# Kernel optimization log

Measured on AMD Instinct MI355X. Metric: run time of the kernel, lower is better.

Reference implementation:

```python
import jax, jax.numpy as jnp
from jax import lax
import numpy as np

SEQ_LEN = 96; PRED_LEN = 96; SIGNAL_LEN = 16; NUM_NODES = 256
EMBED = 128; HIDDEN = 64; K_NN = 8; S_SCALE = 2.0; CHEB_ORDER = 2
MA_K = 3; BATCH = 16
C_FREQ = SIGNAL_LEN // 2 + 1          # 9 rfft bins
M_NODES = NUM_NODES * C_FREQ          # nodes per sample graph


def _sin_posemb(pos, dim):
    half = dim // 2
    freqs = 1.0 / (10000.0 ** (np.arange(half) / half))
    ang = pos[:, None] * freqs[None, :]
    return np.concatenate([np.sin(ang), np.cos(ang)], axis=-1).astype(np.float32)


def setup_inputs():
    key = jax.random.key(0)
    ks = jax.random.split(key, 12)
    x = jax.random.normal(ks[0], (BATCH, SEQ_LEN, NUM_NODES), jnp.float32)
    # Chebyshev (order 2) approx of Haar framelet filters cos(xi/2), sin(xi/2) on [0, pi]
    t = np.linspace(-1.0, 1.0, 201); xi = (t + 1.0) * np.pi / 2.0
    ch = np.polynomial.chebyshev
    approx = np.stack([ch.chebfit(t, np.cos(xi / 2.0), CHEB_ORDER),
                       ch.chebfit(t, np.sin(xi / 2.0), CHEB_ORDER)]).astype(np.float32)
    freq_emb = _sin_posemb(np.arange(C_FREQ, dtype=np.float32) * S_SCALE, EMBED)
    sc = (2.0 / EMBED) ** 0.5
    return dict(
        x=x,
        approx=jnp.asarray(approx),                 # [F=2, K=3]
        theta=jnp.ones((2,), jnp.float32),
        fr_Wr=jax.random.normal(ks[1], (EMBED, EMBED), jnp.float32) * sc,
        fr_Wi=jax.random.normal(ks[2], (EMBED, EMBED), jnp.float32) * sc,
        eo_Wr=jax.random.normal(ks[3], (1, EMBED), jnp.float32) * sc,
        eo_Wi=jax.random.normal(ks[4], (1, EMBED), jnp.float32) * sc,
        freq_emb=jnp.asarray(freq_emb),             # [C, EMBED]
        n1_w=jnp.ones((NUM_NODES,), jnp.float32), n1_b=jnp.zeros((NUM_NODES,), jnp.float32),
        n2_w=jnp.ones((NUM_NODES,), jnp.float32), n2_b=jnp.zeros((NUM_NODES,), jnp.float32),
        W1_w=jax.random.normal(ks[5], (HIDDEN, SEQ_LEN), jnp.float32) * (1.0 / SEQ_LEN ** 0.5),
        W1_b=jnp.zeros((HIDDEN,), jnp.float32),
        W2_w=jax.random.normal(ks[6], (HIDDEN, HIDDEN), jnp.float32) * (1.0 / HIDDEN ** 0.5),
        W2_b=jnp.zeros((HIDDEN,), jnp.float32),
        Wt_w=jax.random.normal(ks[7], (HIDDEN, SEQ_LEN), jnp.float32) * (1.0 / SEQ_LEN ** 0.5),
        Wt_b=jnp.zeros((HIDDEN,), jnp.float32),
        W3_w=jax.random.normal(ks[8], (PRED_LEN, HIDDEN), jnp.float32) * (1.0 / HIDDEN ** 0.5),
        W3_b=jnp.zeros((PRED_LEN,), jnp.float32),
    )


def _clinear(z, Wr, Wi):
    xr, xi = z.real, z.imag
    return lax.complex(xr @ Wr.T - xi @ Wi.T, xr @ Wi.T + xi @ Wr.T)


def _csilu(z):
    return lax.complex(jax.nn.silu(z.real), jax.nn.silu(z.imag))


def _cheb_prop(h, row, col, ew, coeffs):
    # Chebyshev recurrence with A_norm(h) = scatter_add(row, (ew/s) * h[col])
    w = (ew / S_SCALE)[:, None]
    def A(hh):
        return jnp.zeros_like(hh).at[row].add(w * hh[col])
    Tx0 = h
    out = coeffs[0] * Tx0
    Tx1 = -A(Tx0)
    out = out + coeffs[1] * Tx1
    for ki in range(2, CHEB_ORDER + 1):
        Tx2 = -2.0 * A(Tx1) - Tx0
        out = out + coeffs[ki] * Tx2
        Tx0, Tx1 = Tx1, Tx2
    return out


def _knn_one(feat):
    # feat [M, 2] -> symmetrised degree-normalised KNN edges
    sq = jnp.sum(feat * feat, axis=1)
    d2 = sq[:, None] + sq[None, :] - 2.0 * (feat @ feat.T)
    d2 = jnp.where(jnp.eye(M_NODES, dtype=bool), jnp.inf, d2)
    idx = lax.top_k(-d2, K_NN)[1]                      # smallest distances
    src = jnp.repeat(jnp.arange(M_NODES), K_NN)
    dst = idx.reshape(-1)
    r = jnp.concatenate([src, dst])
    c = jnp.concatenate([dst, src])
    deg = jnp.zeros((M_NODES,), jnp.float32).at[r].add(1.0)
    dinv = (deg + 1e-8) ** -0.5
    return r, c, dinv[r] * dinv[c]


def _moving_avg(x):
    pad = MA_K // 2
    front = jnp.repeat(x[:, :1, :], pad, axis=1)
    back = jnp.repeat(x[:, -1:, :], MA_K - 1 - pad, axis=1)
    xp = jnp.concatenate([front, x, back], axis=1)     # (B, T+k-1, N)
    cs = jnp.cumsum(xp, axis=1)
    cs = jnp.concatenate([jnp.zeros_like(cs[:, :1, :]), cs], axis=1)
    return (cs[:, MA_K:, :] - cs[:, :-MA_K, :]) / MA_K  # (B, T, N)


def _inorm(h, w, b):
    mu = jnp.mean(h, axis=-1, keepdims=True)
    var = jnp.mean((h - mu) ** 2, axis=-1, keepdims=True)
    return (h - mu) / jnp.sqrt(var + 1e-5) * w[None, :, None] + b[None, :, None]


def _forward(x, approx, theta, fr_Wr, fr_Wi, eo_Wr, eo_Wi, freq_emb,
             n1_w, n1_b, n2_w, n2_b, W1_w, W1_b, W2_w, W2_b, Wt_w, Wt_b, W3_w, W3_b):
    B, T, N = x.shape
    trend = _moving_avg(x)
    seasonal = x - trend
    S = jnp.fft.rfft(seasonal, n=SIGNAL_LEN, axis=1, norm='ortho')   # (B, C, N) c64
    S_perm = jnp.transpose(S, (0, 2, 1))                             # (B, N, C)
    node_feat = S_perm[..., None] * freq_emb                         # (B, N, C, E) c64
    batch_x = node_feat.reshape(B * M_NODES, EMBED)
    sg = S_perm.reshape(B, M_NODES)
    feat = lax.stop_gradient(jnp.stack([sg.real, sg.imag], axis=-1))  # (B, M, 2)
    rs, cs_, ews = jax.vmap(_knn_one)(feat)
    off = (jnp.arange(B) * M_NODES)[:, None]
    row = (rs + off).reshape(-1)
    col = (cs_ + off).reshape(-1)
    ew = ews.reshape(-1)
    # framelet layer: sum of F filtered Chebyshev propagations
    acc = jnp.zeros_like(batch_x)
    for i in range(approx.shape[0]):
        acc = acc + theta[i] * _cheb_prop(batch_x, row, col, ew, approx[i])
    h = _csilu(_clinear(acc, fr_Wr, fr_Wi))
    S_out = _clinear(h, eo_Wr, eo_Wi).reshape(B, N, C_FREQ)
    H = jnp.fft.irfft(jnp.transpose(S_out, (0, 2, 1)), n=SEQ_LEN, axis=1, norm='ortho')
    H = jnp.transpose(H, (0, 2, 1))                                  # (B, N, T)
    H = jax.nn.silu(_inorm(H, n1_w, n1_b))
    H = H @ W1_w.T + W1_b
    H = jax.nn.silu(_inorm(H, n2_w, n2_b))
    H = H @ W2_w.T + W2_b
    trend_emb = jnp.transpose(trend, (0, 2, 1)) @ Wt_w.T + Wt_b
    return (H + trend_emb) @ W3_w.T + W3_b                           # (B, N, pred_len)


def reference(x, approx, theta, fr_Wr, fr_Wi, eo_Wr, eo_Wi, freq_emb,
              n1_w, n1_b, n2_w, n2_b, W1_w, W1_b, W2_w, W2_b, Wt_w, Wt_b, W3_w, W3_b):
    return _forward(x, approx, theta, fr_Wr, fr_Wi, eo_Wr, eo_Wi, freq_emb,
                    n1_w, n1_b, n2_w, n2_b, W1_w, W1_b, W2_w, W2_b, Wt_w, Wt_b, W3_w, W3_b)
```

## Files before the change

kernel.cpp:

```cpp
#include <hip/hip_runtime.h>
#include <math.h>
#include <float.h>

#define BATCH 16
#define SEQ 96
#define NNODE 256
#define CFREQ 9
#define MNODE (NNODE * CFREQ)
#define BM (BATCH * MNODE)
#define KNN 8
#define EMBED 128
#define HIDDEN 64
#define TN (SEQ * NNODE)
#define KCAP 64
#define NBLK (BM / 256)
#define HROWS 8
#define FEW (CFREQ * EMBED)

__constant__ float COS16[16] = {
    1.0f, 0.9238795325112867f, 0.7071067811865476f, 0.3826834323650898f,
    0.0f, -0.3826834323650898f, -0.7071067811865476f, -0.9238795325112867f,
    -1.0f, -0.9238795325112867f, -0.7071067811865476f, -0.3826834323650898f,
    0.0f, 0.3826834323650898f, 0.7071067811865476f, 0.9238795325112867f};
__constant__ float SIN16[16] = {
    0.0f, 0.3826834323650898f, 0.7071067811865476f, 0.9238795325112867f,
    1.0f, 0.9238795325112867f, 0.7071067811865476f, 0.3826834323650898f,
    0.0f, -0.3826834323650898f, -0.7071067811865476f, -0.9238795325112867f,
    -1.0f, -0.9238795325112867f, -0.7071067811865476f, -0.3826834323650898f};

static __device__ __forceinline__ float silu_f(float x) {
    return x / (1.0f + expf(-x));
}

static __device__ __forceinline__ float rank_h(float2 fj, float xi2, float yi2) {
    float sqj = __fmaf_rn(fj.y, fj.y, __fmul_rn(fj.x, fj.x));
    return __fmaf_rn(xi2, fj.x, __fmaf_rn(yi2, fj.y, sqj));
}

__global__ void __launch_bounds__(256) prep_kernel(
    const float* __restrict__ x, float* __restrict__ S, int* __restrict__ cnt,
    const float* __restrict__ femb, const float* __restrict__ Wr,
    const float* __restrict__ Wi, float* __restrict__ FE) {
    int gid = blockIdx.x * 256 + threadIdx.x;
    if (gid < BM) {
        cnt[gid] = 0;
        int b = gid / MNODE;
        int m = gid - b * MNODE;
        int n = m / CFREQ;
        int c = m - n * CFREQ;
        const float* xb = x + b * TN + n;
        float xv[17];
        #pragma unroll
        for (int t = 0; t < 17; ++t) xv[t] = xb[t * NNODE];
        float re = 0.0f, im = 0.0f;
        #pragma unroll
        for (int t = 0; t < 16; ++t) {
            int tm = t > 0 ? t - 1 : 0;
            float tr = (xv[tm] + xv[t] + xv[t + 1]) * (1.0f / 3.0f);
            float s = xv[t] - tr;
            int k = (c * t) & 15;
            re += s * COS16[k];
            im -= s * SIN16[k];
        }
        S[gid * 2 + 0] = re * 0.25f;
        S[gid * 2 + 1] = im * 0.25f;
    } else {
        int f = gid - BM;
        if (f < FEW) {
            int c = f / EMBED;
            int e = f - c * EMBED;
            float ar = 0.0f, ai = 0.0f;
            for (int k = 0; k < EMBED; ++k) {
                float fv = femb[c * EMBED + k];
                ar += fv * Wr[e * EMBED + k];
                ai += fv * Wi[e * EMBED + k];
            }
            FE[f * 2 + 0] = ar;
            FE[f * 2 + 1] = ai;
        }
    }
}

__global__ void __launch_bounds__(256, 8) knn_kernel(const float* __restrict__ S,
                                                     int* __restrict__ idx, int* __restrict__ cnt) {
    __shared__ float2 f[MNODE];
    __shared__ unsigned long long kbuf[4][KCAP];
    int b = blockIdx.y;
    int tid = threadIdx.x;
    for (int t = tid; t < MNODE; t += 256) {
        f[t] = make_float2(S[(b * MNODE + t) * 2 + 0], S[(b * MNODE + t) * 2 + 1]);
    }
    __syncthreads();
    int wave = tid >> 6, lane = tid & 63;
    int i = blockIdx.x * 4 + wave;
    float2 fi = f[i];
    float xi2 = __fmul_rn(-2.0f, fi.x), yi2 = __fmul_rn(-2.0f, fi.y);
    int lane_i = __builtin_amdgcn_readfirstlane(i & 63);
    int k_i    = __builtin_amdgcn_readfirstlane(i >> 6);

    float h[36];
    float mymin = FLT_MAX;
    #pragma unroll
    for (int k = 0; k < 36; ++k) {
        int j = lane + (k << 6);
        float hh = rank_h(f[j], xi2, yi2);
        if (k == k_i && lane == lane_i) hh = FLT_MAX;
        h[k] = hh;
        mymin = fminf(mymin, hh);
    }
    float g = mymin;
    g = fminf(g, __shfl_xor(g, 1, 64));
    g = fminf(g, __shfl_xor(g, 2, 64));
    g = fminf(g, __shfl_xor(g, 4, 64));
    float T = g;
    T = fmaxf(T, __shfl_xor(T, 8, 64));
    T = fmaxf(T, __shfl_xor(T, 16, 64));
    T = fmaxf(T, __shfl_xor(T, 32, 64));
    unsigned long long* mybuf = kbuf[wave];
    const unsigned long long lmask = (1ull << lane) - 1ull;
    int total = 0;
    #pragma unroll
    for (int k = 0; k < 36; ++k) {
        bool pred = h[k] <= T;
        unsigned long long mask = __ballot(pred);
        if (pred) {
            int pos = total + (int)__popcll(mask & lmask);
            if (pos < KCAP) {
                unsigned int bits = __float_as_uint(h[k]);
                if (bits == 0x80000000u) bits = 0u;
                unsigned int s = bits ^ (unsigned int)(((int)bits >> 31) | 0x80000000);
                mybuf[pos] = ((unsigned long long)s << 32) | (unsigned int)(lane + (k << 6));
            }
        }
        total += (int)__popcll(mask);
    }

    if (total >= KNN && total <= KCAP) {
        int padded = (total + 7) & ~7;
        if (lane < padded - total) mybuf[total + lane] = ~0ull;
        for (int p = lane; p < total; p += 64) {
            unsigned long long mykey = mybuf[p];
            int rank = 0;
            for (int q = 0; q < padded; q += 8) {
                const ulonglong2* bp = (const ulonglong2*)&mybuf[q];
                ulonglong2 a = bp[0], b2 = bp[1], c2 = bp[2], d2 = bp[3];
                rank += (int)(a.x  < mykey) + (int)(a.y  < mykey)
                      + (int)(b2.x < mykey) + (int)(b2.y < mykey)
                      + (int)(c2.x < mykey) + (int)(c2.y < mykey)
                      + (int)(d2.x < mykey) + (int)(d2.y < mykey);
            }
            if (rank < KNN) {
                int j = (int)(unsigned int)(mykey & 0xFFFFFFFFull);
                idx[(b * MNODE + i) * KNN + rank] = j;
                atomicAdd(&cnt[b * MNODE + j], 1);
            }
        }
    } else {
        const unsigned long long SENT = ~0ull;
        unsigned long long k0 = SENT, k1 = SENT, k2 = SENT, k3 = SENT,
                           k4 = SENT, k5 = SENT, k6 = SENT, k7 = SENT;
        #pragma unroll
        for (int k = 0; k < 36; ++k) {
            unsigned int bits = __float_as_uint(h[k]);
            if (bits == 0x80000000u) bits = 0u;
            unsigned int s = bits ^ (unsigned int)(((int)bits >> 31) | 0x80000000);
            unsigned long long key = ((unsigned long long)s << 32) | (unsigned int)(lane + (k << 6));
            if (key < k7) {
                k7 = key;
                if (k7 < k6) { unsigned long long t = k6; k6 = k7; k7 = t; }
                if (k6 < k5) { unsigned long long t = k5; k5 = k6; k6 = t; }
                if (k5 < k4) { unsigned long long t = k4; k4 = k5; k5 = t; }
                if (k4 < k3) { unsigned long long t = k3; k3 = k4; k4 = t; }
                if (k3 < k2) { unsigned long long t = k2; k2 = k3; k3 = t; }
                if (k2 < k1) { unsigned long long t = k1; k1 = k2; k2 = t; }
                if (k1 < k0) { unsigned long long t = k0; k0 = k1; k1 = t; }
            }
        }
        unsigned long long mywin = 0;
        #pragma unroll
        for (int r = 0; r < KNN; ++r) {
            unsigned long long hh = k0;
            #pragma unroll
            for (int off = 32; off > 0; off >>= 1) {
                unsigned long long o = __shfl_xor(hh, off, 64);
                if (o < hh) hh = o;
            }
            if (lane == r) mywin = hh;
            if (k0 == hh) {
                k0 = k1; k1 = k2; k2 = k3; k3 = k4; k4 = k5; k5 = k6; k6 = k7; k7 = SENT;
            }
        }
        if (lane < KNN) {
            int j = (int)(unsigned int)(mywin & 0xFFFFFFFFull);
            idx[(b * MNODE + i) * KNN + lane] = j;
            atomicAdd(&cnt[b * MNODE + j], 1);
        }
    }
}

__global__ void __launch_bounds__(256) dinv_scanblk_kernel(
    const int* __restrict__ cnt, const float* __restrict__ S,
    float* __restrict__ dinv, float* __restrict__ PS, int* __restrict__ bsum) {
    __shared__ int wsum[4];
    int tid = threadIdx.x;
    int gid = blockIdx.x * 256 + tid;
    int c = cnt[gid];
    float deg = (float)(KNN + c);
    float dv = 1.0f / sqrtf(deg + 1e-8f);
    dinv[gid] = dv;
    PS[gid * 2 + 0] = dv * S[gid * 2 + 0];
    PS[gid * 2 + 1] = dv * S[gid * 2 + 1];
    int s = c;
    #pragma unroll
    for (int off = 32; off > 0; off >>= 1) s += __shfl_down(s, off, 64);
    if ((tid & 63) == 0) wsum[tid >> 6] = s;
    __syncthreads();
    if (tid == 0) bsum[blockIdx.x] = wsum[0] + wsum[1] + wsum[2] + wsum[3];
}

__global__ void __launch_bounds__(256) scan_apply_kernel(const int* __restrict__ cnt,
                                                         const int* __restrict__ bsum,
                                                         int2* __restrict__ oc,
                                                         int* __restrict__ fptr) {
    __shared__ int wsum[4];
    __shared__ int sbase[4];
    int tid = threadIdx.x;
    int lane = tid & 63, wv = tid >> 6;
    int bb = 0;
    if (tid < NBLK && tid < (int)blockIdx.x) bb = bsum[tid];
    #pragma unroll
    for (int off = 32; off > 0; off >>= 1) bb += __shfl_down(bb, off, 64);
    if (lane == 0) sbase[wv] = bb;
    int gid = blockIdx.x * 256 + tid;
    int v = cnt[gid];
    int x = v;
    #pragma unroll
    for (int off = 1; off < 64; off <<= 1) {
        int y = __shfl_up(x, off, 64);
        if (lane >= off) x += y;
    }
    if (lane == 63) wsum[wv] = x;
    __syncthreads();
    int base = sbase[0] + sbase[1] + sbase[2] + sbase[3];
    for (int w = 0; w < wv; ++w) base += wsum[w];
    int o = base + x - v;
    oc[gid] = make_int2(o, v);
    fptr[gid] = o;
}

__global__ void fill_kernel(const int* __restrict__ idx,
                            int* __restrict__ fptr, int* __restrict__ rev) {
    int gid = blockIdx.x * blockDim.x + threadIdx.x;
    if (gid >= BM * KNN) return;
    int b = gid / (MNODE * KNN);
    int rem = gid - b * (MNODE * KNN);
    int i = rem / KNN;
    int gj = b * MNODE + idx[gid];
    int pos = atomicAdd(&fptr[gj], 1);
    rev[pos] = b * MNODE + i;
}

__global__ void __launch_bounds__(256) gather1_kernel(
    const int* __restrict__ idx, const int2* __restrict__ oc,
    const int* __restrict__ rev, const float* __restrict__ dinv, const float* __restrict__ PS,
    float* __restrict__ zA, float* __restrict__ zAw) {
    int gid = blockIdx.x * blockDim.x + threadIdx.x;
    if (gid >= BM * CFREQ) return;
    int gi = gid / CFREQ;
    int c = gid - gi * CFREQ;
    int b = gi / MNODE;
    float ax = 0.0f, ay = 0.0f;
    #pragma unroll
    for (int k = 0; k < KNN; ++k) {
        int gj = b * MNODE + idx[gi * KNN + k];
        bool m = (gj % CFREQ) == c;
        float2 p = ((const float2*)PS)[gj];
        ax += m ? p.x : 0.0f;
        ay += m ? p.y : 0.0f;
    }
    int2 ocv = oc[gi];
    int o = ocv.x, e = o + ocv.y;
    for (int p_ = o; p_ < e; ++p_) {
        int gk = rev[p_];
        bool m = (gk % CFREQ) == c;
        float2 p = ((const float2*)PS)[gk];
        ax += m ? p.x : 0.0f;
        ay += m ? p.y : 0.0f;
    }
    float dv = dinv[gi];
    float s = dv * 0.5f;
    float zx = s * ax, zy = s * ay;
    zA[gid * 2 + 0] = zx;
    zA[gid * 2 + 1] = zy;
    zAw[gid * 2 + 0] = dv * zx;
    zAw[gid * 2 + 1] = dv * zy;
}

__global__ void __launch_bounds__(256) gather2_kernel(
    const int* __restrict__ idx, const int2* __restrict__ oc,
    const int* __restrict__ rev, const float* __restrict__ dinv, const float* __restrict__ zAw,
    float* __restrict__ zB) {
    int gid = blockIdx.x * blockDim.x + threadIdx.x;
    if (gid >= BM * CFREQ) return;
    int gi = gid / CFREQ;
    int c = gid - gi * CFREQ;
    int b = gi / MNODE;
    float ax = 0.0f, ay = 0.0f;
    #pragma unroll
    for (int k = 0; k < KNN; ++k) {
        int gj = b * MNODE + idx[gi * KNN + k];
        float2 v = ((const float2*)zAw)[gj * CFREQ + c];
        ax += v.x;
        ay += v.y;
    }
    int2 ocv = oc[gi];
    int o = ocv.x, e = o + ocv.y;
    for (int p = o; p < e; ++p) {
        int gk = rev[p];
        float2 v = ((const float2*)zAw)[gk * CFREQ + c];
        ax += v.x;
        ay += v.y;
    }
    float s = dinv[gi] * 0.5f;
    zB[gid * 2 + 0] = s * ax;
    zB[gid * 2 + 1] = s * ay;
}

__global__ void __launch_bounds__(256) rowproj_kernel(
    const float* __restrict__ S, const float* __restrict__ zA, const float* __restrict__ zB,
    const float* __restrict__ FE, const float* __restrict__ eoWr, const float* __restrict__ eoWi,
    const float* __restrict__ theta, const float* __restrict__ approx,
    float* __restrict__ Sout) {
    int wave = threadIdx.x >> 6;
    int lane = threadIdx.x & 63;
    int r = blockIdx.x * 4 + wave;
    if (r >= BM) return;
    float a0 = theta[0] * approx[0] + theta[1] * approx[3];
    float a1 = theta[0] * approx[1] + theta[1] * approx[4];
    float a2 = theta[0] * approx[2] + theta[1] * approx[5];
    float ca = a0 - a2, cb = -a1, cc = 2.0f * a2;
    int cr = r % CFREQ;
    float sr = S[r * 2 + 0], si = S[r * 2 + 1];
    int e1 = lane + 64;
    float ur0 = 0.0f, ui0 = 0.0f, ur1 = 0.0f, ui1 = 0.0f;
    #pragma unroll
    for (int c = 0; c < CFREQ; ++c) {
        float zr = cb * zA[(r * CFREQ + c) * 2 + 0] + cc * zB[(r * CFREQ + c) * 2 + 0];
        float zi = cb * zA[(r * CFREQ + c) * 2 + 1] + cc * zB[(r * CFREQ + c) * 2 + 1];
        if (c == cr) { zr += ca * sr; zi += ca * si; }
        float fr0 = FE[(c * EMBED + lane) * 2 + 0], fi0 = FE[(c * EMBED + lane) * 2 + 1];
        float fr1 = FE[(c * EMBED + e1) * 2 + 0],  fi1 = FE[(c * EMBED + e1) * 2 + 1];
        ur0 += zr * fr0 - zi * fi0;  ui0 += zr * fi0 + zi * fr0;
        ur1 += zr * fr1 - zi * fi1;  ui1 += zr * fi1 + zi * fr1;
    }
    float hr0 = silu_f(ur0), hi0 = silu_f(ui0);
    float hr1 = silu_f(ur1), hi1 = silu_f(ui1);
    float wr0 = eoWr[lane], wi0 = eoWi[lane], wr1 = eoWr[e1], wi1 = eoWi[e1];
    float p = hr0 * wr0 - hi0 * wi0 + hr1 * wr1 - hi1 * wi1;
    float q = hr0 * wi0 + hi0 * wr0 + hr1 * wi1 + hi1 * wr1;
    #pragma unroll
    for (int off = 32; off > 0; off >>= 1) {
        p += __shfl_down(p, off, 64);
        q += __shfl_down(q, off, 64);
    }
    if (lane == 0) {
        Sout[r * 2 + 0] = p;
        Sout[r * 2 + 1] = q;
    }
}

__global__ void __launch_bounds__(512) head_kernel(
    const float* __restrict__ Sout, const float* __restrict__ x,
    const float* __restrict__ n1w, const float* __restrict__ n1b,
    const float* __restrict__ n2w, const float* __restrict__ n2b,
    const float* __restrict__ W1w, const float* __restrict__ W1b,
    const float* __restrict__ W2w, const float* __restrict__ W2b,
    const float* __restrict__ Wtw, const float* __restrict__ Wtb,
    const float* __restrict__ W3w, const float* __restrict__ W3b,
    float* __restrict__ out) {
    __shared__ float tabc[96], tabs[96];
    __shared__ float srow[HROWS][18];
    __shared__ float tbuf[HROWS][96];
    __shared__ float hraw[HROWS][96];
    __shared__ float sH[HROWS][96];
    __shared__ float h2[HROWS][64];
    __shared__ float s3[HROWS][64];
    __shared__ float red[HROWS][2];
    __shared__ float wbuf[6240];
    int tid = threadIdx.x;
    int wave = tid >> 6, lane = tid & 63;
    int bn0 = blockIdx.x * HROWS;
    if (tid < 96) {
        double a = 6.283185307179586476925286766559 * (double)tid / 96.0;
        tabc[tid] = (float)cos(a);
        tabs[tid] = (float)sin(a);
    }
    for (int i = tid; i < HROWS * 96; i += 512) {
        int g = i / 96, t = i - g * 96;
        int bn = bn0 + g;
        hraw[g][t] = x[(bn >> 8) * TN + t * NNODE + (bn & 255)];
    }
    if (tid < HROWS * 18) {
        int g = tid / 18, k = tid - g * 18;
        srow[g][k] = Sout[(bn0 + g) * 18 + k];
    }
    __syncthreads();
    for (int i = tid; i < HROWS * 96; i += 512) {
        int g = i / 96, t = i - g * 96;
        int tm = t > 0 ? t - 1 : 0;
        int tp = t < SEQ - 1 ? t + 1 : SEQ - 1;
        tbuf[g][t] = (hraw[g][tm] + hraw[g][t] + hraw[g][tp]) * (1.0f / 3.0f);
    }
    __syncthreads();
    for (int i = tid; i < HROWS * 96; i += 512) {
        int g = i / 96, t = i - g * 96;
        float acc = srow[g][0];
        #pragma unroll
        for (int c = 1; c < CFREQ; ++c) {
            int k = (c * t) % 96;
            acc += 2.0f * (srow[g][2 * c] * tabc[k] - srow[g][2 * c + 1] * tabs[k]);
        }
        hraw[g][t] = acc * 0.10206207261596575f;
    }
    __syncthreads();
    {
        float v = hraw[wave][lane] + ((lane < 32) ? hraw[wave][64 + lane] : 0.0f);
        #pragma unroll
        for (int off = 32; off > 0; off >>= 1) v += __shfl_down(v, off, 64);
        if (lane == 0) red[wave][0] = v * (1.0f / 96.0f);
    }
    __syncthreads();
    {
        float mu = red[wave][0];
        float d0 = hraw[wave][lane] - mu;
        float v = d0 * d0;
        if (lane < 32) { float d1 = hraw[wave][64 + lane] - mu; v += d1 * d1; }
        #pragma unroll
        for (int off = 32; off > 0; off >>= 1) v += __shfl_down(v, off, 64);
        if (lane == 0) red[wave][1] = v * (1.0f / 96.0f);
    }
    __syncthreads();
    for (int i = tid; i < HROWS * 96; i += 512) {
        int g = i / 96, t = i - g * 96;
        int n = (bn0 + g) & 255;
        float xn = (hraw[g][t] - red[g][0]) / sqrtf(red[g][1] + 1e-5f) * n1w[n] + n1b[n];
        sH[g][t] = silu_f(xn);
    }
    for (int i = tid; i < HIDDEN * 96; i += 512) {
        int rr = i / 96;
        wbuf[rr * 97 + (i - rr * 96)] = W1w[i];
    }
    __syncthreads();
    float v1;
    {
        float acc = W1b[lane];
        #pragma unroll 8
        for (int t = 0; t < 96; ++t) acc += sH[wave][t] * wbuf[lane * 97 + t];
        v1 = acc;
    }
    {
        float s = v1;
        #pragma unroll
        for (int off = 32; off > 0; off >>= 1) s += __shfl_down(s, off, 64);
        s = __shfl(s, 0, 64);
        float mu2 = s * (1.0f / 64.0f);
        float d = v1 - mu2;
        float vs = d * d;
        #pragma unroll
        for (int off = 32; off > 0; off >>= 1) vs += __shfl_down(vs, off, 64);
        vs = __shfl(vs, 0, 64);
        float var2 = vs * (1.0f / 64.0f);
        int n = (bn0 + wave) & 255;
        float xn = (v1 - mu2) / sqrtf(var2 + 1e-5f) * n2w[n] + n2b[n];
        h2[wave][lane] = silu_f(xn);
    }
    __syncthreads();
    for (int i = tid; i < HIDDEN * HIDDEN; i += 512) {
        wbuf[(i >> 6) * 65 + (i & 63)] = W2w[i];
    }
    __syncthreads();
    float v3;
    {
        float acc = W2b[lane];
        #pragma unroll 8
        for (int h = 0; h < 64; ++h) acc += h2[wave][h] * wbuf[lane * 65 + h];
        v3 = acc;
    }
    __syncthreads();
    for (int i = tid; i < HIDDEN * 96; i += 512) {
        int rr = i / 96;
        wbuf[rr * 97 + (i - rr * 96)] = Wtw[i];
    }
    __syncthreads();
    {
        float acc = Wtb[lane];
        #pragma unroll 8
        for (int t = 0; t < 96; ++t) acc += tbuf[wave][t] * wbuf[lane * 97 + t];
        s3[wave][lane] = v3 + acc;
    }
    __syncthreads();
    for (int i = tid; i < 96 * HIDDEN; i += 512) {
        wbuf[(i >> 6) * 65 + (i & 63)] = W3w[i];
    }
    __syncthreads();
    for (int i = tid; i < HROWS * 96; i += 512) {
        int g = i / 96, t = i - g * 96;
        float acc = W3b[t];
        #pragma unroll 8
        for (int h = 0; h < 64; ++h) acc += s3[g][h] * wbuf[t * 65 + h];
        out[(bn0 + g) * 96 + t] = acc;
    }
}

extern "C" void kernel_launch(void* const* d_in, const int* in_sizes, int n_in,
                              void* d_out, int out_size, void* d_ws, size_t ws_size,
                              hipStream_t stream) {
    const float* x     = (const float*)d_in[0];
    const float* approx= (const float*)d_in[1];
    const float* theta = (const float*)d_in[2];
    const float* frWr  = (const float*)d_in[3];
    const float* frWi  = (const float*)d_in[4];
    const float* eoWr  = (const float*)d_in[5];
    const float* eoWi  = (const float*)d_in[6];
    const float* femb  = (const float*)d_in[7];
    const float* n1w   = (const float*)d_in[8];
    const float* n1b   = (const float*)d_in[9];
    const float* n2w   = (const float*)d_in[10];
    const float* n2b   = (const float*)d_in[11];
    const float* W1w   = (const float*)d_in[12];
    const float* W1b   = (const float*)d_in[13];
    const float* W2w   = (const float*)d_in[14];
    const float* W2b   = (const float*)d_in[15];
    const float* Wtw   = (const float*)d_in[16];
    const float* Wtb   = (const float*)d_in[17];
    const float* W3w   = (const float*)d_in[18];
    const float* W3b   = (const float*)d_in[19];
    float* out = (float*)d_out;

    char* ws = (char*)d_ws;
    size_t off = 0;
    auto alloc = [&](size_t bytes) -> void* {
        void* p = ws + off;
        off = (off + bytes + 255) & ~(size_t)255;
        return p;
    };
    float* S     = (float*)alloc((size_t)BM * 2 * 4);
    int*   idx   = (int*)  alloc((size_t)BM * KNN * 4);
    float* dinv  = (float*)alloc((size_t)BM * 4);
    float* PS    = (float*)alloc((size_t)BM * 2 * 4);
    float* FE    = (float*)alloc((size_t)FEW * 2 * 4);
    float* Sout  = (float*)alloc((size_t)BM * 2 * 4);
    int2*  oc    = (int2*) alloc((size_t)BM * 8);
    int*   rev   = (int*)  alloc((size_t)BM * KNN * 4);
    float* zA    = (float*)alloc((size_t)BM * CFREQ * 2 * 4);
    float* zAw   = (float*)alloc((size_t)BM * CFREQ * 2 * 4);
    float* zB    = (float*)alloc((size_t)BM * CFREQ * 2 * 4);
    int*   bsum  = (int*)  alloc((size_t)NBLK * 4);
    int*   cnt   = (int*)  alloc((size_t)BM * 4);
    int*   fptr  = (int*)  alloc((size_t)BM * 4);

    prep_kernel<<<(BM + FEW + 255) / 256, 256, 0, stream>>>(x, S, cnt, femb, frWr, frWi, FE);
    knn_kernel<<<dim3(MNODE / 4, BATCH), 256, 0, stream>>>(S, idx, cnt);
    dinv_scanblk_kernel<<<NBLK, 256, 0, stream>>>(cnt, S, dinv, PS, bsum);
    scan_apply_kernel<<<NBLK, 256, 0, stream>>>(cnt, bsum, oc, fptr);
    fill_kernel<<<(BM * KNN + 255) / 256, 256, 0, stream>>>(idx, fptr, rev);
    gather1_kernel<<<(BM * CFREQ + 255) / 256, 256, 0, stream>>>(idx, oc, rev, dinv, PS, zA, zAw);
    gather2_kernel<<<(BM * CFREQ + 255) / 256, 256, 0, stream>>>(idx, oc, rev, dinv, zAw, zB);
    rowproj_kernel<<<BM / 4, 256, 0, stream>>>(S, zA, zB, FE, eoWr, eoWi, theta, approx, Sout);
    head_kernel<<<BATCH * NNODE / HROWS, 512, 0, stream>>>(Sout, x, n1w, n1b, n2w, n2b,
                                                           W1w, W1b, W2w, W2b, Wtw, Wtb, W3w, W3b, out);
}
```

Baseline: 248.2 us.

## Merge scan kernels via atomic base, fold Chebyshev combine into gather2, widen head

The two-pass block scan becomes a single kernel. Each block takes its base offset from a global atomic counter, which is zeroed in prep_kernel. The CSR segments therefore land in arbitrary block order, but each node's segment stays contiguous. gather2 now writes the combined Chebyshev term cb*zA + cc*zB directly, so rowproj reads one array instead of two. The head kernel processes 16 rows per 1024-thread block, and the kNN ballot prefix uses mbcnt intrinsics. The aim is to cut one launch, one full intermediate read, and some per-block weight reloads, at the cost of larger head blocks and lower occupancy flexibility.

```diff
diff --git a/kernel.cpp b/kernel.cpp
--- a/kernel.cpp
+++ b/kernel.cpp
@@ -14,7 +14,7 @@
 #define TN (SEQ * NNODE)
 #define KCAP 64
 #define NBLK (BM / 256)
-#define HROWS 8
+#define HROWS 16
 #define FEW (CFREQ * EMBED)
 
 __constant__ float COS16[16] = {
@@ -37,12 +37,19 @@
     return __fmaf_rn(xi2, fj.x, __fmaf_rn(yi2, fj.y, sqj));
 }
 
+static __device__ __forceinline__ int lane_prefix(unsigned long long mask) {
+    return (int)__builtin_amdgcn_mbcnt_hi(
+        (unsigned int)(mask >> 32),
+        __builtin_amdgcn_mbcnt_lo((unsigned int)mask, 0u));
+}
+
 __global__ void __launch_bounds__(256) prep_kernel(
     const float* __restrict__ x, float* __restrict__ S, int* __restrict__ cnt,
     const float* __restrict__ femb, const float* __restrict__ Wr,
-    const float* __restrict__ Wi, float* __restrict__ FE) {
+    const float* __restrict__ Wi, float* __restrict__ FE, int* __restrict__ gtotal) {
     int gid = blockIdx.x * 256 + threadIdx.x;
     if (gid < BM) {
+        if (gid == 0) *gtotal = 0;
         cnt[gid] = 0;
         int b = gid / MNODE;
         int m = gid - b * MNODE;
@@ -117,14 +124,13 @@
     T = fmaxf(T, __shfl_xor(T, 16, 64));
     T = fmaxf(T, __shfl_xor(T, 32, 64));
     unsigned long long* mybuf = kbuf[wave];
-    const unsigned long long lmask = (1ull << lane) - 1ull;
     int total = 0;
     #pragma unroll
     for (int k = 0; k < 36; ++k) {
         bool pred = h[k] <= T;
         unsigned long long mask = __ballot(pred);
         if (pred) {
-            int pos = total + (int)__popcll(mask & lmask);
+            int pos = total + lane_prefix(mask);
             if (pos < KCAP) {
                 unsigned int bits = __float_as_uint(h[k]);
                 if (bits == 0x80000000u) bits = 0u;
@@ -198,41 +204,21 @@
     }
 }
 
-__global__ void __launch_bounds__(256) dinv_scanblk_kernel(
+__global__ void __launch_bounds__(256) scan_kernel(
     const int* __restrict__ cnt, const float* __restrict__ S,
-    float* __restrict__ dinv, float* __restrict__ PS, int* __restrict__ bsum) {
+    float* __restrict__ dinv, float* __restrict__ PS,
+    int* __restrict__ gtotal, int2* __restrict__ oc, int* __restrict__ fptr) {
     __shared__ int wsum[4];
+    __shared__ int sbase;
     int tid = threadIdx.x;
+    int lane = tid & 63, wv = tid >> 6;
     int gid = blockIdx.x * 256 + tid;
-    int c = cnt[gid];
-    float deg = (float)(KNN + c);
+    int v = cnt[gid];
+    float deg = (float)(KNN + v);
     float dv = 1.0f / sqrtf(deg + 1e-8f);
     dinv[gid] = dv;
     PS[gid * 2 + 0] = dv * S[gid * 2 + 0];
     PS[gid * 2 + 1] = dv * S[gid * 2 + 1];
-    int s = c;
-    #pragma unroll
-    for (int off = 32; off > 0; off >>= 1) s += __shfl_down(s, off, 64);
-    if ((tid & 63) == 0) wsum[tid >> 6] = s;
-    __syncthreads();
-    if (tid == 0) bsum[blockIdx.x] = wsum[0] + wsum[1] + wsum[2] + wsum[3];
-}
-
-__global__ void __launch_bounds__(256) scan_apply_kernel(const int* __restrict__ cnt,
-                                                         const int* __restrict__ bsum,
-                                                         int2* __restrict__ oc,
-                                                         int* __restrict__ fptr) {
-    __shared__ int wsum[4];
-    __shared__ int sbase[4];
-    int tid = threadIdx.x;
-    int lane = tid & 63, wv = tid >> 6;
-    int bb = 0;
-    if (tid < NBLK && tid < (int)blockIdx.x) bb = bsum[tid];
-    #pragma unroll
-    for (int off = 32; off > 0; off >>= 1) bb += __shfl_down(bb, off, 64);
-    if (lane == 0) sbase[wv] = bb;
-    int gid = blockIdx.x * 256 + tid;
-    int v = cnt[gid];
     int x = v;
     #pragma unroll
     for (int off = 1; off < 64; off <<= 1) {
@@ -241,7 +227,9 @@
     }
     if (lane == 63) wsum[wv] = x;
     __syncthreads();
-    int base = sbase[0] + sbase[1] + sbase[2] + sbase[3];
+    if (tid == 0) sbase = atomicAdd(gtotal, wsum[0] + wsum[1] + wsum[2] + wsum[3]);
+    __syncthreads();
+    int base = sbase;
     for (int w = 0; w < wv; ++w) base += wsum[w];
     int o = base + x - v;
     oc[gid] = make_int2(o, v);
@@ -298,10 +286,15 @@
 
 __global__ void __launch_bounds__(256) gather2_kernel(
     const int* __restrict__ idx, const int2* __restrict__ oc,
-    const int* __restrict__ rev, const float* __restrict__ dinv, const float* __restrict__ zAw,
-    float* __restrict__ zB) {
+    const int* __restrict__ rev, const float* __restrict__ dinv,
+    const float* __restrict__ zA, const float* __restrict__ zAw,
+    const float* __restrict__ theta, const float* __restrict__ approx,
+    float* __restrict__ zF) {
     int gid = blockIdx.x * blockDim.x + threadIdx.x;
     if (gid >= BM * CFREQ) return;
+    float a1 = theta[0] * approx[1] + theta[1] * approx[4];
+    float a2 = theta[0] * approx[2] + theta[1] * approx[5];
+    float cb = -a1, cc = 2.0f * a2;
     int gi = gid / CFREQ;
     int c = gid - gi * CFREQ;
     int b = gi / MNODE;
@@ -322,12 +315,13 @@
         ay += v.y;
     }
     float s = dinv[gi] * 0.5f;
-    zB[gid * 2 + 0] = s * ax;
-    zB[gid * 2 + 1] = s * ay;
+    float2 za = ((const float2*)zA)[gid];
+    zF[gid * 2 + 0] = cb * za.x + cc * (s * ax);
+    zF[gid * 2 + 1] = cb * za.y + cc * (s * ay);
 }
 
 __global__ void __launch_bounds__(256) rowproj_kernel(
-    const float* __restrict__ S, const float* __restrict__ zA, const float* __restrict__ zB,
+    const float* __restrict__ S, const float* __restrict__ zF,
     const float* __restrict__ FE, const float* __restrict__ eoWr, const float* __restrict__ eoWi,
     const float* __restrict__ theta, const float* __restrict__ approx,
     float* __restrict__ Sout) {
@@ -336,17 +330,16 @@
     int r = blockIdx.x * 4 + wave;
     if (r >= BM) return;
     float a0 = theta[0] * approx[0] + theta[1] * approx[3];
-    float a1 = theta[0] * approx[1] + theta[1] * approx[4];
     float a2 = theta[0] * approx[2] + theta[1] * approx[5];
-    float ca = a0 - a2, cb = -a1, cc = 2.0f * a2;
+    float ca = a0 - a2;
     int cr = r % CFREQ;
     float sr = S[r * 2 + 0], si = S[r * 2 + 1];
     int e1 = lane + 64;
     float ur0 = 0.0f, ui0 = 0.0f, ur1 = 0.0f, ui1 = 0.0f;
     #pragma unroll
     for (int c = 0; c < CFREQ; ++c) {
-        float zr = cb * zA[(r * CFREQ + c) * 2 + 0] + cc * zB[(r * CFREQ + c) * 2 + 0];
-        float zi = cb * zA[(r * CFREQ + c) * 2 + 1] + cc * zB[(r * CFREQ + c) * 2 + 1];
+        float2 zf = ((const float2*)zF)[r * CFREQ + c];
+        float zr = zf.x, zi = zf.y;
         if (c == cr) { zr += ca * sr; zi += ca * si; }
         float fr0 = FE[(c * EMBED + lane) * 2 + 0], fi0 = FE[(c * EMBED + lane) * 2 + 1];
         float fr1 = FE[(c * EMBED + e1) * 2 + 0],  fi1 = FE[(c * EMBED + e1) * 2 + 1];
@@ -369,7 +362,7 @@
     }
 }
 
-__global__ void __launch_bounds__(512) head_kernel(
+__global__ void __launch_bounds__(1024) head_kernel(
     const float* __restrict__ Sout, const float* __restrict__ x,
     const float* __restrict__ n1w, const float* __restrict__ n1b,
     const float* __restrict__ n2w, const float* __restrict__ n2b,
@@ -395,7 +388,7 @@
         tabc[tid] = (float)cos(a);
         tabs[tid] = (float)sin(a);
     }
-    for (int i = tid; i < HROWS * 96; i += 512) {
+    for (int i = tid; i < HROWS * 96; i += 1024) {
         int g = i / 96, t = i - g * 96;
         int bn = bn0 + g;
         hraw[g][t] = x[(bn >> 8) * TN + t * NNODE + (bn & 255)];
@@ -405,14 +398,14 @@
         srow[g][k] = Sout[(bn0 + g) * 18 + k];
     }
     __syncthreads();
-    for (int i = tid; i < HROWS * 96; i += 512) {
+    for (int i = tid; i < HROWS * 96; i += 1024) {
         int g = i / 96, t = i - g * 96;
         int tm = t > 0 ? t - 1 : 0;
         int tp = t < SEQ - 1 ? t + 1 : SEQ - 1;
         tbuf[g][t] = (hraw[g][tm] + hraw[g][t] + hraw[g][tp]) * (1.0f / 3.0f);
     }
     __syncthreads();
-    for (int i = tid; i < HROWS * 96; i += 512) {
+    for (int i = tid; i < HROWS * 96; i += 1024) {
         int g = i / 96, t = i - g * 96;
         float acc = srow[g][0];
         #pragma unroll
@@ -440,13 +433,13 @@
         if (lane == 0) red[wave][1] = v * (1.0f / 96.0f);
     }
     __syncthreads();
-    for (int i = tid; i < HROWS * 96; i += 512) {
+    for (int i = tid; i < HROWS * 96; i += 1024) {
         int g = i / 96, t = i - g * 96;
         int n = (bn0 + g) & 255;
         float xn = (hraw[g][t] - red[g][0]) / sqrtf(red[g][1] + 1e-5f) * n1w[n] + n1b[n];
         sH[g][t] = silu_f(xn);
     }
-    for (int i = tid; i < HIDDEN * 96; i += 512) {
+    for (int i = tid; i < HIDDEN * 96; i += 1024) {
         int rr = i / 96;
         wbuf[rr * 97 + (i - rr * 96)] = W1w[i];
     }
@@ -475,7 +468,7 @@
         h2[wave][lane] = silu_f(xn);
     }
     __syncthreads();
-    for (int i = tid; i < HIDDEN * HIDDEN; i += 512) {
+    for (int i = tid; i < HIDDEN * HIDDEN; i += 1024) {
         wbuf[(i >> 6) * 65 + (i & 63)] = W2w[i];
     }
     __syncthreads();
@@ -487,7 +480,7 @@
         v3 = acc;
     }
     __syncthreads();
-    for (int i = tid; i < HIDDEN * 96; i += 512) {
+    for (int i = tid; i < HIDDEN * 96; i += 1024) {
         int rr = i / 96;
         wbuf[rr * 97 + (i - rr * 96)] = Wtw[i];
     }
@@ -499,11 +492,11 @@
         s3[wave][lane] = v3 + acc;
     }
     __syncthreads();
-    for (int i = tid; i < 96 * HIDDEN; i += 512) {
+    for (int i = tid; i < 96 * HIDDEN; i += 1024) {
         wbuf[(i >> 6) * 65 + (i & 63)] = W3w[i];
     }
     __syncthreads();
-    for (int i = tid; i < HROWS * 96; i += 512) {
+    for (int i = tid; i < HROWS * 96; i += 1024) {
         int g = i / 96, t = i - g * 96;
         float acc = W3b[t];
         #pragma unroll 8
@@ -554,19 +547,19 @@
     int*   rev   = (int*)  alloc((size_t)BM * KNN * 4);
     float* zA    = (float*)alloc((size_t)BM * CFREQ * 2 * 4);
     float* zAw   = (float*)alloc((size_t)BM * CFREQ * 2 * 4);
-    float* zB    = (float*)alloc((size_t)BM * CFREQ * 2 * 4);
-    int*   bsum  = (int*)  alloc((size_t)NBLK * 4);
+    float* zF    = (float*)alloc((size_t)BM * CFREQ * 2 * 4);
     int*   cnt   = (int*)  alloc((size_t)BM * 4);
     int*   fptr  = (int*)  alloc((size_t)BM * 4);
-
-    prep_kernel<<<(BM + FEW + 255) / 256, 256, 0, stream>>>(x, S, cnt, femb, frWr, frWi, FE);
+    int*   gtotal= (int*)  alloc(256);
+
+    prep_kernel<<<(BM + FEW + 255) / 256, 256, 0, stream>>>(x, S, cnt, femb, frWr, frWi, FE, gtotal);
     knn_kernel<<<dim3(MNODE / 4, BATCH), 256, 0, stream>>>(S, idx, cnt);
-    dinv_scanblk_kernel<<<NBLK, 256, 0, stream>>>(cnt, S, dinv, PS, bsum);
-    scan_apply_kernel<<<NBLK, 256, 0, stream>>>(cnt, bsum, oc, fptr);
+    scan_kernel<<<NBLK, 256, 0, stream>>>(cnt, S, dinv, PS, gtotal, oc, fptr);
     fill_kernel<<<(BM * KNN + 255) / 256, 256, 0, stream>>>(idx, fptr, rev);
     gather1_kernel<<<(BM * CFREQ + 255) / 256, 256, 0, stream>>>(idx, oc, rev, dinv, PS, zA, zAw);
-    gather2_kernel<<<(BM * CFREQ + 255) / 256, 256, 0, stream>>>(idx, oc, rev, dinv, zAw, zB);
-    rowproj_kernel<<<BM / 4, 256, 0, stream>>>(S, zA, zB, FE, eoWr, eoWi, theta, approx, Sout);
-    head_kernel<<<BATCH * NNODE / HROWS, 512, 0, stream>>>(Sout, x, n1w, n1b, n2w, n2b,
-                                                           W1w, W1b, W2w, W2b, Wtw, Wtb, W3w, W3b, out);
-}
+    gather2_kernel<<<(BM * CFREQ + 255) / 256, 256, 0, stream>>>(idx, oc, rev, dinv, zA, zAw,
+                                                                 theta, approx, zF);
+    rowproj_kernel<<<BM / 4, 256, 0, stream>>>(S, zF, FE, eoWr, eoWi, theta, approx, Sout);
+    head_kernel<<<BATCH * NNODE / HROWS, 1024, 0, stream>>>(Sout, x, n1w, n1b, n2w, n2b,
+                                                            W1w, W1b, W2w, W2b, Wtw, Wtb, W3w, W3b, out);
+}
```

New measurement: 241.9 us. -2.5%, faster.
